# Kernel optimization log

Hardware: AMD Instinct MI355X
Metric: run time of the kernel (lower is better)

## Reference

```python
import jax, jax.numpy as jnp
import numpy as np

B, K, V = 32, 2048, 60000
D, H, L, NB = 512, 8, 4, 5
DH, M = D // H, 256  # dim_head, num random features
EPS_K = 1e-4


def _ln(x, g, b, eps=1e-5):
    mu = x.mean(-1, keepdims=True)
    var = ((x - mu) ** 2).mean(-1, keepdims=True)
    return (x - mu) / jnp.sqrt(var + eps) * g + b


def _favor_feats(x, proj, is_query):
    # FAVOR+ positive softmax-kernel features (lucidrains performer)
    dn = x.shape[-1] ** -0.25
    xd = x * dn
    dd = jnp.einsum('bhnd,md->bhnm', xd, proj)
    diag = 0.5 * jnp.sum(xd * xd, -1, keepdims=True)
    mx = jnp.max(dd, -1, keepdims=True) if is_query else jnp.max(dd)
    return (proj.shape[0] ** -0.5) * (jnp.exp(dd - diag - mx) + EPS_K)


def _orth_proj(m, d, rng):
    # gaussian orthogonal random matrix (scaling=0: chi row norms)
    blocks = []
    for _ in range(-(-m // d)):
        q, _ = np.linalg.qr(rng.standard_normal((d, d)))
        blocks.append(q.T)
    mat = np.concatenate(blocks)[:m]
    mult = np.linalg.norm(rng.standard_normal((m, d)), axis=1)
    return (mult[:, None] * mat).astype(np.float32)


def setup_inputs() -> dict:
    rng = np.random.default_rng(0)
    w = lambda *s: jnp.asarray(rng.standard_normal(s).astype(np.float32) * 0.02)
    return dict(
        expr=jnp.asarray(rng.random((B, K)).astype(np.float32)),
        coords=jnp.asarray(rng.standard_normal((B, 2)).astype(np.float32)),
        gene_ids=jnp.arange(K, dtype=jnp.int32),
        gene_table=w(V, D), pos_table=w(K, D), value_table=w(NB, D),
        sp_w=w(2, D), sp_b=jnp.zeros(D), sp_ln_g=jnp.ones(D), sp_ln_b=jnp.zeros(D),
        ln1_g=jnp.ones((L, D)), ln1_b=jnp.zeros((L, D)),
        qw=w(L, D, D), qb=jnp.zeros((L, D)), kw=w(L, D, D), kb=jnp.zeros((L, D)),
        vw=w(L, D, D), vb=jnp.zeros((L, D)), ow=w(L, D, D), ob=jnp.zeros((L, D)),
        proj=jnp.asarray(np.stack([_orth_proj(M, DH, rng) for _ in range(L)])),
        ln2_g=jnp.ones((L, D)), ln2_b=jnp.zeros((L, D)),
        ff1_w=w(L, D, 4 * D), ff1_b=jnp.zeros((L, 4 * D)),
        ff2_w=w(L, 4 * D, D), ff2_b=jnp.zeros((L, D)),
        cq_w=w(D, D), cq_b=jnp.zeros(D), ck_w=w(D, D), ck_b=jnp.zeros(D),
        cv_w=w(D, D), cv_b=jnp.zeros(D), co_w=w(D, D), co_b=jnp.zeros(D),
    )


def reference(expr, coords, gene_ids, gene_table, pos_table, value_table,
              sp_w, sp_b, sp_ln_g, sp_ln_b, ln1_g, ln1_b, qw, qb, kw, kb,
              vw, vb, ow, ob, proj, ln2_g, ln2_b, ff1_w, ff1_b, ff2_w, ff2_b,
              cq_w, cq_b, ck_w, ck_b, cv_w, cv_b, co_w, co_b):
    b, k = expr.shape
    bins = jnp.clip((expr * NB).astype(jnp.int32), 0, NB - 1)
    gene_embeds = gene_table[gene_ids][None] + pos_table[None, :k] + value_table[bins]
    sp = jax.nn.gelu(_ln(coords @ sp_w + sp_b, sp_ln_g, sp_ln_b), approximate=False)
    x = jnp.concatenate([sp[:, None, :], gene_embeds], axis=1)  # (B, K+1, D)
    n = k + 1
    for l in range(L):
        h = _ln(x, ln1_g[l], ln1_b[l])
        q = (h @ qw[l] + qb[l]).reshape(b, n, H, DH).transpose(0, 2, 1, 3)
        kk = (h @ kw[l] + kb[l]).reshape(b, n, H, DH).transpose(0, 2, 1, 3)
        v = (h @ vw[l] + vb[l]).reshape(b, n, H, DH).transpose(0, 2, 1, 3)
        qp = _favor_feats(q, proj[l], True)   # (b,h,n,M)
        kp = _favor_feats(kk, proj[l], False)
        dinv = 1.0 / jnp.einsum('bhnm,bhm->bhn', qp, kp.sum(axis=2))
        ctx = jnp.einsum('bhnm,bhnd->bhmd', kp, v)
        o = jnp.einsum('bhnm,bhmd->bhnd', qp, ctx) * dinv[..., None]
        o = o.transpose(0, 2, 1, 3).reshape(b, n, D)
        x = x + (o @ ow[l] + ob[l])
        h = _ln(x, ln2_g[l], ln2_b[l])
        x = x + jax.nn.gelu(h @ ff1_w[l] + ff1_b[l], approximate=False) @ ff2_w[l] + ff2_b[l]
    qc = x[:, :1] @ cq_w + cq_b
    kc = x[:, 1:] @ ck_w + ck_b
    vc = x[:, 1:] @ cv_w + cv_b
    attn = jax.nn.softmax(jnp.einsum('bqd,bkd->bqk', qc, kc) / (D ** 0.5), axis=-1)
    pooled = jnp.einsum('bqk,bkd->bqd', attn, vc)[:, 0]
    return pooled @ co_w + co_b
```

## Files before the change

### kernel.cpp

```cpp
#include <hip/hip_runtime.h>
#include <hip/hip_bf16.h>

#define BB 32
#define KK 2048
#define NTOK 2049
#define DD 512
#define NH 8
#define DHD 64
#define NL 4
#define MM 256
#define RTOT (BB*NTOK)
#define HROWS (RTOT/2)
#define DN 0.35355339059327373f
#define RM 0.0625f
#define EPSK 1e-4f

typedef __attribute__((ext_vector_type(8))) short bf16x8;
typedef __attribute__((ext_vector_type(4))) float f32x4;

__device__ __forceinline__ float wsum(float v) {
#pragma unroll
  for (int o = 32; o; o >>= 1) v += __shfl_xor(v, o);
  return v;
}
__device__ __forceinline__ float wmax(float v) {
#pragma unroll
  for (int o = 32; o; o >>= 1) v = fmaxf(v, __shfl_xor(v, o));
  return v;
}
__device__ __forceinline__ float gelu1(float v) {
  return 0.5f * v * (1.0f + erff(v * 0.70710678118654752f));
}
__device__ __forceinline__ float b2f(unsigned short u) {
  union { unsigned int i; float f; } w; w.i = ((unsigned int)u) << 16; return w.f;
}
__device__ __forceinline__ unsigned short f2b(float f) {
  union { float f; unsigned int i; } w; w.f = f;
  unsigned int r = w.i + 0x7FFFu + ((w.i >> 16) & 1u);
  return (unsigned short)(r >> 16);
}
__device__ __forceinline__ float4 ld4(const float* p) { return *(const float4*)p; }
__device__ __forceinline__ float4 ld4(const unsigned short* p) {
  ushort4 u = *(const ushort4*)p;
  return make_float4(b2f(u.x), b2f(u.y), b2f(u.z), b2f(u.w));
}
__device__ __forceinline__ void st4(float* p, float4 v) { *(float4*)p = v; }
__device__ __forceinline__ void st4(unsigned short* p, float4 v) {
  ushort4 u; u.x = f2b(v.x); u.y = f2b(v.y); u.z = f2b(v.z); u.w = f2b(v.w);
  *(ushort4*)p = u;
}
__device__ __forceinline__ bf16x8 ld8s(const unsigned short* p) {
  union { ushort4 u[2]; bf16x8 v; } w;
  w.u[0] = *(const ushort4*)p;
  w.u[1] = *(const ushort4*)(p + 4);
  return w.v;
}
__device__ __forceinline__ void gload16(const void* g, void* l) {
  __builtin_amdgcn_global_load_lds(
      (const __attribute__((address_space(1))) void*)g,
      (__attribute__((address_space(3))) void*)l, 16, 0, 0);
}

__global__ void sentinel_k(float* out, int n) {
  int i = blockIdx.x * 256 + threadIdx.x;
  if (i < n) out[i] = 12345.0f;
}

__global__ void biaspack_k(const float* __restrict__ a, const float* __restrict__ bsrc,
                           float* __restrict__ dst) {
  int i = threadIdx.x;
  dst[i] = a[i]; dst[i + 256] = a[i + 256];
  dst[512 + i] = bsrc[i]; dst[768 + i] = bsrc[i + 256];
}
__global__ void biaspack3_k(const float* __restrict__ a, const float* __restrict__ bsrc,
                            const float* __restrict__ c, float* __restrict__ dst) {
  int i = threadIdx.x;
  dst[i] = a[i]; dst[i + 256] = a[i + 256];
  dst[512 + i] = bsrc[i]; dst[768 + i] = bsrc[i + 256];
  dst[1024 + i] = c[i]; dst[1280 + i] = c[i + 256];
}

__global__ __launch_bounds__(256) void wcvt_k(const float* __restrict__ W,
    unsigned short* __restrict__ Wt, int Kd, int Cols) {
  __shared__ float Ls[64][65];
  int tid = threadIdx.x;
  int n0 = blockIdx.x * 64, k0 = blockIdx.y * 64;
  int kr = tid >> 2, nseg = (tid & 3) << 4;
#pragma unroll
  for (int u = 0; u < 4; ++u) {
    float4 v = *(const float4*)(W + (size_t)(k0 + kr) * Cols + n0 + nseg + u * 4);
    *(float4*)&Ls[kr][nseg + u * 4] = v;
  }
  __syncthreads();
  int nr = tid >> 2, kseg = (tid & 3) << 4;
  unsigned int pk[8];
#pragma unroll
  for (int i = 0; i < 8; ++i) {
    unsigned short lo = f2b(Ls[kseg + 2 * i][nr]);
    unsigned short hi = f2b(Ls[kseg + 2 * i + 1][nr]);
    pk[i] = (unsigned int)lo | ((unsigned int)hi << 16);
  }
  unsigned short* dst = Wt + (size_t)(n0 + nr) * Kd + k0 + kseg;
  ((uint4*)dst)[0] = make_uint4(pk[0], pk[1], pk[2], pk[3]);
  ((uint4*)dst)[1] = make_uint4(pk[4], pk[5], pk[6], pk[7]);
}

__global__ __launch_bounds__(256) void embed_k(const float* __restrict__ expr,
    const int* __restrict__ gene_ids, const float* __restrict__ gene_table,
    const float* __restrict__ pos_table, const float* __restrict__ value_tab,
    unsigned short* __restrict__ x) {
  int tok = blockIdx.x * 2 + (threadIdx.x >> 7);
  int t = threadIdx.x & 127;
  int b = tok >> 11;
  int k = tok & 2047;
  float e = expr[tok];
  int bin = (int)(e * 5.0f);
  bin = bin < 0 ? 0 : (bin > 4 ? 4 : bin);
  int g = gene_ids[k];
  float4 a = ((const float4*)(gene_table + (size_t)g * DD))[t];
  float4 p = ((const float4*)(pos_table + (size_t)k * DD))[t];
  float4 vv = ((const float4*)(value_tab + (size_t)bin * DD))[t];
  float4 r;
  r.x = a.x + p.x + vv.x; r.y = a.y + p.y + vv.y;
  r.z = a.z + p.z + vv.z; r.w = a.w + p.w + vv.w;
  st4(x + ((size_t)b * NTOK + 1 + k) * DD + t * 4, r);
}

__global__ __launch_bounds__(256) void sp_k(const float* __restrict__ coords,
    const float* __restrict__ sp_w, const float* __restrict__ sp_b,
    const float* __restrict__ g, const float* __restrict__ bb,
    unsigned short* __restrict__ x) {
  int b = blockIdx.x, t = threadIdx.x;
  __shared__ float red[8];
  float c0 = coords[2 * b], c1 = coords[2 * b + 1];
  float v0 = fmaf(c0, sp_w[t],       fmaf(c1, sp_w[512 + t], sp_b[t]));
  float v1 = fmaf(c0, sp_w[t + 256], fmaf(c1, sp_w[768 + t], sp_b[t + 256]));
  float s = wsum(v0 + v1);
  int wid = t >> 6;
  if ((t & 63) == 0) red[wid] = s;
  __syncthreads();
  float mu = (red[0] + red[1] + red[2] + red[3]) * (1.0f / 512.0f);
  float d0 = v0 - mu, d1 = v1 - mu;
  float s2 = wsum(d0 * d0 + d1 * d1);
  if ((t & 63) == 0) red[4 + wid] = s2;
  __syncthreads();
  float var = (red[4] + red[5] + red[6] + red[7]) * (1.0f / 512.0f);
  float rs = rsqrtf(var + 1e-5f);
  float y0 = d0 * rs * g[t] + bb[t];
  float y1 = d1 * rs * g[t + 256] + bb[t + 256];
  x[(size_t)b * NTOK * DD + t] = f2b(gelu1(y0));
  x[(size_t)b * NTOK * DD + t + 256] = f2b(gelu1(y1));
}

__global__ __launch_bounds__(128) void ln_k(const unsigned short* __restrict__ x,
    const float* __restrict__ gamma, const float* __restrict__ beta,
    unsigned short* __restrict__ h) {
  size_t row = blockIdx.x;
  int t = threadIdx.x;
  float4 v = ld4(x + row * DD + t * 4);
  float s = v.x + v.y + v.z + v.w;
  float s2 = v.x * v.x + v.y * v.y + v.z * v.z + v.w * v.w;
  __shared__ float red[4];
  float ws1 = wsum(s), ws2 = wsum(s2);
  int wid = t >> 6;
  if ((t & 63) == 0) { red[wid * 2] = ws1; red[wid * 2 + 1] = ws2; }
  __syncthreads();
  float S = red[0] + red[2], S2 = red[1] + red[3];
  float mu = S * (1.0f / 512.0f);
  float var = S2 * (1.0f / 512.0f) - mu * mu;
  float rs = rsqrtf(var + 1e-5f);
  float4 gm = ((const float4*)gamma)[t], bt = ((const float4*)beta)[t];
  float4 o;
  o.x = (v.x - mu) * rs * gm.x + bt.x;
  o.y = (v.y - mu) * rs * gm.y + bt.y;
  o.z = (v.z - mu) * rs * gm.z + bt.z;
  o.w = (v.w - mu) * rs * gm.w + bt.w;
  st4(h + row * DD + t * 4, o);
}

template <typename TC, int FLAGS>
__global__ __launch_bounds__(256) void gemm_bb(const unsigned short* __restrict__ A, long lda,
    const unsigned short* __restrict__ Wt, const float* __restrict__ bias,
    TC* __restrict__ C, int ldc, int R, int Kd) {
  __shared__ unsigned short Sh[128 * 136];
  unsigned short* As = Sh;
  unsigned short* Bs = Sh + 128 * 64;
  const int tid = threadIdx.x;
  const int lane = tid & 63;
  const int w = tid >> 6;
  const int wr = w >> 1, wc = w & 1;
  const int nwg = gridDim.x * gridDim.y;
  const int orig = blockIdx.y * gridDim.x + blockIdx.x;
  const int qd = nwg >> 3, rm = nwg & 7;
  const int xcd = orig & 7, idx = orig >> 3;
  const int wg = (xcd < rm ? xcd * (qd + 1) : rm * (qd + 1) + (xcd - rm) * qd) + idx;
  const int rblk = (wg / gridDim.x) << 7;
  const int cblk = (wg % gridDim.x) << 7;
  const int m0 = lane & 15, kb = lane >> 4;
  const int lrow8 = lane >> 3;
  const int csw = (((lane & 7) ^ lrow8) << 3);
  f32x4 acc[4][4] = {};
  for (int k0 = 0; k0 < Kd; k0 += 64) {
#pragma unroll
    for (int rd = 0; rd < 4; ++rd) {
      int rg = w * 32 + rd * 8;
      int gra = rblk + rg + lrow8; if (gra >= R) gra = R - 1;
      gload16(A  + (size_t)gra * lda + k0 + csw, &As[rg * 64]);
      gload16(Wt + (size_t)(cblk + rg + lrow8) * Kd + k0 + csw, &Bs[rg * 64]);
    }
    __syncthreads();
    bf16x8 af[2][4], bfr[2][4];
#pragma unroll
    for (int ks = 0; ks < 2; ++ks) {
      int c = (ks << 2) | kb;
#pragma unroll
      for (int mi = 0; mi < 4; ++mi) {
        int ar = wr * 64 + mi * 16 + m0;
        af[ks][mi] = *(const bf16x8*)&As[ar * 64 + ((c ^ (ar & 7)) << 3)];
        int br = wc * 64 + mi * 16 + m0;
        bfr[ks][mi] = *(const bf16x8*)&Bs[br * 64 + ((c ^ (br & 7)) << 3)];
      }
    }
#pragma unroll
    for (int ks = 0; ks < 2; ++ks)
#pragma unroll
      for (int mi = 0; mi < 4; ++mi)
#pragma unroll
        for (int ni = 0; ni < 4; ++ni)
          acc[mi][ni] = __builtin_amdgcn_mfma_f32_16x16x32_bf16(af[ks][mi], bfr[ks][ni], acc[mi][ni], 0, 0, 0);
    __syncthreads();
  }
  const int lrow4 = (lane >> 4) << 2, lcol = lane & 15;
  if constexpr (sizeof(TC) == 2 && (FLAGS & 2) == 0) {
#pragma unroll
    for (int mi = 0; mi < 4; ++mi)
#pragma unroll
      for (int reg = 0; reg < 4; ++reg) {
        int rloc = wr * 64 + mi * 16 + lrow4 + reg;
#pragma unroll
        for (int ni = 0; ni < 4; ++ni) {
          int cloc = wc * 64 + ni * 16 + lcol;
          float v = acc[mi][ni][reg] + bias[cblk + cloc];
          if constexpr ((FLAGS & 1) != 0) v = gelu1(v);
          Sh[rloc * 136 + cloc] = f2b(v);
        }
      }
    __syncthreads();
    int rl = tid >> 1;
    int row = rblk + rl;
    if (row < R) {
      unsigned short* cp = (unsigned short*)C + (size_t)row * ldc + cblk;
#pragma unroll
      for (int u = 0; u < 8; ++u) {
        int c = (tid & 1) * 8 + u * 16;
        *(uint4*)(cp + c) = *(const uint4*)&Sh[rl * 136 + c];
      }
    }
  } else {
    float* Sf = (float*)Sh;
#pragma unroll
    for (int p = 0; p < 2; ++p) {
      if (wr == p) {
#pragma unroll
        for (int mi = 0; mi < 4; ++mi)
#pragma unroll
          for (int reg = 0; reg < 4; ++reg) {
            int rloc = mi * 16 + lrow4 + reg;
#pragma unroll
            for (int ni = 0; ni < 4; ++ni) {
              int cloc = wc * 64 + ni * 16 + lcol;
              float v = acc[mi][ni][reg] + bias[cblk + cloc];
              if constexpr ((FLAGS & 1) != 0) v = gelu1(v);
              Sf[rloc * 132 + cloc] = v;
            }
          }
      }
      __syncthreads();
      int rl = tid >> 2;
      int row = rblk + p * 64 + rl;
      if (row < R) {
        if constexpr (sizeof(TC) == 4) {
          float* cp = (float*)C + (size_t)row * ldc + cblk;
#pragma unroll
          for (int u = 0; u < 8; ++u) {
            int c = (tid & 3) * 4 + u * 16;
            float4 nv = *(const float4*)&Sf[rl * 132 + c];
            if constexpr ((FLAGS & 2) != 0) {
              float4 old = *(const float4*)(cp + c);
              nv.x += old.x; nv.y += old.y; nv.z += old.z; nv.w += old.w;
            }
            *(float4*)(cp + c) = nv;
          }
        } else {
          unsigned short* cp = (unsigned short*)C + (size_t)row * ldc + cblk;
#pragma unroll
          for (int u = 0; u < 8; ++u) {
            int c = (tid & 3) * 4 + u * 16;
            float4 nv = *(const float4*)&Sf[rl * 132 + c];
            ushort4 old = *(const ushort4*)(cp + c);
            ushort4 nw;
            nw.x = f2b(nv.x + b2f(old.x)); nw.y = f2b(nv.y + b2f(old.y));
            nw.z = f2b(nv.z + b2f(old.z)); nw.w = f2b(nv.w + b2f(old.w));
            *(ushort4*)(cp + c) = nw;
          }
        }
      }
      __syncthreads();
    }
  }
}

template <typename TA, typename TC>
__global__ __launch_bounds__(256) void gemm_t(const TA* __restrict__ A, long lda,
    const float* __restrict__ W, const float* __restrict__ bias,
    TC* __restrict__ C, int ldc, int R, int Kd, int Cols) {
  __shared__ float As[16][68];
  __shared__ float Ws[16][64];
  int tid = threadIdx.x;
  int tx = tid & 15, ty = tid >> 4;
  int rblk = blockIdx.y << 6, cblk = blockIdx.x << 6;
  float acc[4][4] = {};
  int lr = tid >> 2, lk = (tid & 3) << 2;
  int wk = tid >> 4, wcc = (tid & 15) << 2;
  int gra = rblk + lr;
  for (int k0 = 0; k0 < Kd; k0 += 16) {
    float4 av = make_float4(0.f, 0.f, 0.f, 0.f);
    if (gra < R) av = ld4(A + (size_t)gra * lda + k0 + lk);
    As[lk][lr] = av.x; As[lk + 1][lr] = av.y; As[lk + 2][lr] = av.z; As[lk + 3][lr] = av.w;
    *(float4*)&Ws[wk][wcc] = *(const float4*)(W + (size_t)(k0 + wk) * Cols + cblk + wcc);
    __syncthreads();
#pragma unroll
    for (int p = 0; p < 16; ++p) {
      float4 a4 = *(const float4*)&As[p][ty << 2];
      float4 b4 = *(const float4*)&Ws[p][tx << 2];
      acc[0][0] = fmaf(a4.x, b4.x, acc[0][0]); acc[0][1] = fmaf(a4.x, b4.y, acc[0][1]);
      acc[0][2] = fmaf(a4.x, b4.z, acc[0][2]); acc[0][3] = fmaf(a4.x, b4.w, acc[0][3]);
      acc[1][0] = fmaf(a4.y, b4.x, acc[1][0]); acc[1][1] = fmaf(a4.y, b4.y, acc[1][1]);
      acc[1][2] = fmaf(a4.y, b4.z, acc[1][2]); acc[1][3] = fmaf(a4.y, b4.w, acc[1][3]);
      acc[2][0] = fmaf(a4.z, b4.x, acc[2][0]); acc[2][1] = fmaf(a4.z, b4.y, acc[2][1]);
      acc[2][2] = fmaf(a4.z, b4.z, acc[2][2]); acc[2][3] = fmaf(a4.z, b4.w, acc[2][3]);
      acc[3][0] = fmaf(a4.w, b4.x, acc[3][0]); acc[3][1] = fmaf(a4.w, b4.y, acc[3][1]);
      acc[3][2] = fmaf(a4.w, b4.z, acc[3][2]); acc[3][3] = fmaf(a4.w, b4.w, acc[3][3]);
    }
    __syncthreads();
  }
  int gcb = cblk + (tx << 2);
  float4 bi = *(const float4*)(bias + gcb);
#pragma unroll
  for (int i = 0; i < 4; ++i) {
    int gr = rblk + (ty << 2) + i;
    if (gr < R) {
      float4 val;
      val.x = acc[i][0] + bi.x; val.y = acc[i][1] + bi.y;
      val.z = acc[i][2] + bi.z; val.w = acc[i][3] + bi.w;
      TC* cp = C + (size_t)gr * ldc + gcb;
      st4(cp, val);
    }
  }
}

__global__ __launch_bounds__(256) void kmax_k(const unsigned short* __restrict__ kv,
    const unsigned short* __restrict__ projb, float* __restrict__ bmax) {
  int orig = blockIdx.y * gridDim.x + blockIdx.x;
  int wg = ((orig & 7) << 7) + (orig >> 3);
  int bh = wg >> 2, gy = wg & 3;
  int b = bh >> 3, hh = bh & 7;
  int tid = threadIdx.x;
  int lane = tid & 63, w = tid >> 6;
  int m0 = lane & 15, kb = lane >> 4;
  __shared__ float red[4];
  bf16x8 bp[4][2];
#pragma unroll
  for (int nf = 0; nf < 4; ++nf)
#pragma unroll
    for (int ks = 0; ks < 2; ++ks)
      bp[nf][ks] = *(const bf16x8*)(projb + (size_t)(w * 64 + nf * 16 + m0) * 64 + ks * 32 + kb * 8);
  const unsigned short* kvb = kv + (size_t)b * NTOK * 1536 + hh * 64;
  float mx = -1e30f;
  for (int t = gy; t < 65; t += 4) {
    int n0 = t * 32;
    bf16x8 aq[2][2];
#pragma unroll
    for (int mi = 0; mi < 2; ++mi) {
      int n = n0 + mi * 16 + m0; if (n >= NTOK) n = NTOK - 1;
#pragma unroll
      for (int ks = 0; ks < 2; ++ks)
        aq[mi][ks] = *(const bf16x8*)(kvb + (size_t)n * 1536 + ks * 32 + kb * 8);
    }
    f32x4 da[2][4] = {};
#pragma unroll
    for (int ks = 0; ks < 2; ++ks)
#pragma unroll
      for (int mi = 0; mi < 2; ++mi)
#pragma unroll
        for (int nf = 0; nf < 4; ++nf)
          da[mi][nf] = __builtin_amdgcn_mfma_f32_16x16x32_bf16(aq[mi][ks], bp[nf][ks], da[mi][nf], 0, 0, 0);
#pragma unroll
    for (int mi = 0; mi < 2; ++mi)
#pragma unroll
      for (int nf = 0; nf < 4; ++nf)
#pragma unroll
        for (int r = 0; r < 4; ++r)
          mx = fmaxf(mx, da[mi][nf][r]);
  }
  mx *= DN;
  mx = wmax(mx);
  if ((tid & 63) == 0) red[tid >> 6] = mx;
  __syncthreads();
  if (tid == 0)
    bmax[(size_t)bh * 4 + gy] = fmaxf(fmaxf(red[0], red[1]), fmaxf(red[2], red[3]));
}

__global__ __launch_bounds__(256) void maxred_k(const float* __restrict__ in, int n,
                                                float* __restrict__ out) {
  float m = -1e30f;
  for (int i = threadIdx.x; i < n; i += 256) m = fmaxf(m, in[i]);
  m = wmax(m);
  __shared__ float red[4];
  if ((threadIdx.x & 63) == 0) red[threadIdx.x >> 6] = m;
  __syncthreads();
  if (threadIdx.x == 0) out[0] = fmaxf(fmaxf(red[0], red[1]), fmaxf(red[2], red[3]));
}

__global__ __launch_bounds__(256) void k2_k(const unsigned short* __restrict__ kv,
    const unsigned short* __restrict__ projb,
    const float* __restrict__ kmaxg, unsigned short* __restrict__ ctxTb,
    float* __restrict__ kpsum) {
  int orig = blockIdx.y * gridDim.x + blockIdx.x;
  int wg = ((orig & 7) << 7) + (orig >> 3);
  int bh = wg >> 2, mg = wg & 3;
  int b = bh >> 3, hh = bh & 7;
  int tid = threadIdx.x;
  int lane = tid & 63, w = tid >> 6;
  int m0 = lane & 15, kb = lane >> 4;
  __shared__ __align__(16) unsigned short kpT[64 * 44];
  __shared__ __align__(16) unsigned short VT[64 * 44];
  float kmax = kmaxg[0];
  bf16x8 bp[2];
#pragma unroll
  for (int ks = 0; ks < 2; ++ks)
    bp[ks] = *(const bf16x8*)(projb + (size_t)(mg * 64 + w * 16 + m0) * 64 + ks * 32 + kb * 8);
  f32x4 acc[4] = {};
  float ksum = 0.f;
  int dv = tid & 63, tq = tid >> 6;
  const unsigned short* kvb = kv + (size_t)b * NTOK * 1536 + hh * 64;
  for (int t = 0; t < 65; ++t) {
    int n0 = t * 32;
    int tlim = NTOK - n0; if (tlim > 32) tlim = 32;
    __syncthreads();
    {
      unsigned int pk[4];
#pragma unroll
      for (int j = 0; j < 8; ++j) {
        int n = n0 + tq * 8 + j; if (n >= NTOK) n = NTOK - 1;
        unsigned int v = kvb[(size_t)n * 1536 + 512 + dv];
        if (j & 1) pk[j >> 1] |= v << 16; else pk[j >> 1] = v;
      }
      *(uint2*)&VT[dv * 44 + tq * 8]     = make_uint2(pk[0], pk[1]);
      *(uint2*)&VT[dv * 44 + tq * 8 + 4] = make_uint2(pk[2], pk[3]);
    }
    bf16x8 aq[2][2];
    float dg[2];
#pragma unroll
    for (int mi = 0; mi < 2; ++mi) {
      int n = n0 + mi * 16 + m0; if (n >= NTOK) n = NTOK - 1;
      float s = 0.f;
#pragma unroll
      for (int ks = 0; ks < 2; ++ks) {
        aq[mi][ks] = *(const bf16x8*)(kvb + (size_t)n * 1536 + ks * 32 + kb * 8);
        const unsigned short* ap = (const unsigned short*)&aq[mi][ks];
#pragma unroll
        for (int j = 0; j < 8; ++j) { float v = b2f(ap[j]); s = fmaf(v, v, s); }
      }
      s += __shfl_xor(s, 16);
      s += __shfl_xor(s, 32);
      dg[mi] = 0.5f * DN * DN * s;
    }
    f32x4 da[2] = {};
#pragma unroll
    for (int ks = 0; ks < 2; ++ks)
#pragma unroll
      for (int mi = 0; mi < 2; ++mi)
        da[mi] = __builtin_amdgcn_mfma_f32_16x16x32_bf16(aq[mi][ks], bp[ks], da[mi], 0, 0, 0);
#pragma unroll
    for (int mi = 0; mi < 2; ++mi) {
      unsigned int pk[2];
#pragma unroll
      for (int r = 0; r < 4; ++r) {
        float dval = __shfl(dg[mi], (kb << 2) | r);
        int tt = mi * 16 + (kb << 2) + r;
        float kp = 0.f;
        if (tt < tlim)
          kp = RM * (__expf(da[mi][r] * DN - dval - kmax) + EPSK);
        ksum += kp;
        unsigned int h = (unsigned int)f2b(kp);
        if (r & 1) pk[r >> 1] |= h << 16; else pk[r >> 1] = h;
      }
      *(uint2*)&kpT[(w * 16 + m0) * 44 + mi * 16 + (kb << 2)] = make_uint2(pk[0], pk[1]);
    }
    __syncthreads();
    bf16x8 af = ld8s(&kpT[(w * 16 + m0) * 44 + kb * 8]);
#pragma unroll
    for (int di = 0; di < 4; ++di) {
      bf16x8 bfv = ld8s(&VT[(di * 16 + m0) * 44 + kb * 8]);
      acc[di] = __builtin_amdgcn_mfma_f32_16x16x32_bf16(af, bfv, acc[di], 0, 0, 0);
    }
  }
  ksum += __shfl_xor(ksum, 16);
  ksum += __shfl_xor(ksum, 32);
  if (kb == 0) kpsum[(size_t)bh * MM + mg * 64 + w * 16 + m0] = ksum;
  unsigned short* cT = ctxTb + (size_t)bh * (64 * 256);
#pragma unroll
  for (int di = 0; di < 4; ++di)
#pragma unroll
    for (int r = 0; r < 4; ++r) {
      int m = mg * 64 + w * 16 + (kb << 2) + r;
      int d = di * 16 + m0;
      cT[d * 256 + m] = f2b(acc[di][r]);
    }
}

__global__ __launch_bounds__(256) void qfeat_k(unsigned short* __restrict__ kv,
    const unsigned short* __restrict__ projb,
    const unsigned short* __restrict__ ctxTb,
    const float* __restrict__ kpsum) {
  int orig = blockIdx.y * gridDim.x + blockIdx.x;
  int wg = ((orig & 7) * 416) + (orig >> 3);
  int bh = wg / 13, gy = wg % 13;
  int b = bh >> 3, hh = bh & 7;
  int tid = threadIdx.x;
  int lane = tid & 63, w = tid >> 6;
  int m0 = lane & 15, kb = lane >> 4;
  __shared__ float ddl[32 * 266];
  __shared__ unsigned short Pb[32 * 264];
  __shared__ float ksum_s[256];
  __shared__ float diag_s[32];
  __shared__ float dinv_s[32];
  ksum_s[tid] = kpsum[(size_t)bh * MM + tid];
  bf16x8 bp[4][2], bc[8];
#pragma unroll
  for (int nf = 0; nf < 4; ++nf)
#pragma unroll
    for (int ks = 0; ks < 2; ++ks)
      bp[nf][ks] = *(const bf16x8*)(projb + (size_t)(w * 64 + nf * 16 + m0) * 64 + ks * 32 + kb * 8);
  const unsigned short* cT = ctxTb + (size_t)bh * (64 * 256);
#pragma unroll
  for (int ks = 0; ks < 8; ++ks)
    bc[ks] = *(const bf16x8*)(cT + (size_t)(w * 16 + m0) * 256 + ks * 32 + kb * 8);
  unsigned short* kvb = kv + (size_t)b * NTOK * 1536 + hh * 64;
  int t8 = tid >> 3, q8 = tid & 7;
  for (int t = gy; t < 65; t += 13) {
    int n0 = t * 32;
    int tlim = NTOK - n0; if (tlim > 32) tlim = 32;
    bf16x8 aq[2][2];
#pragma unroll
    for (int mi = 0; mi < 2; ++mi) {
      int n = n0 + mi * 16 + m0; if (n >= NTOK) n = NTOK - 1;
#pragma unroll
      for (int ks = 0; ks < 2; ++ks)
        aq[mi][ks] = *(const bf16x8*)(kvb + (size_t)n * 1536 + 1024 + ks * 32 + kb * 8);
    }
#pragma unroll
    for (int mi = 0; mi < 2; ++mi) {
      float s = 0.f;
      const unsigned short* ap = (const unsigned short*)&aq[mi][0];
#pragma unroll
      for (int j = 0; j < 16; ++j) { float v = b2f(ap[j]); s = fmaf(v, v, s); }
      s += __shfl_xor(s, 16); s += __shfl_xor(s, 32);
      if (w == 0 && kb == 0) diag_s[mi * 16 + m0] = 0.5f * DN * DN * s;
    }
    f32x4 da[2][4] = {};
#pragma unroll
    for (int ks = 0; ks < 2; ++ks)
#pragma unroll
      for (int mi = 0; mi < 2; ++mi)
#pragma unroll
        for (int nf = 0; nf < 4; ++nf)
          da[mi][nf] = __builtin_amdgcn_mfma_f32_16x16x32_bf16(aq[mi][ks], bp[nf][ks], da[mi][nf], 0, 0, 0);
#pragma unroll
    for (int mi = 0; mi < 2; ++mi)
#pragma unroll
      for (int nf = 0; nf < 4; ++nf)
#pragma unroll
        for (int r = 0; r < 4; ++r)
          ddl[(mi * 16 + kb * 4 + r) * 266 + w * 64 + nf * 16 + m0] = da[mi][nf][r] * DN;
    __syncthreads();
    float mx = -1e30f;
    if (t8 < tlim) {
      for (int j = 0; j < 32; ++j) mx = fmaxf(mx, ddl[t8 * 266 + q8 + 8 * j]);
    }
    mx = fmaxf(mx, __shfl_xor(mx, 1));
    mx = fmaxf(mx, __shfl_xor(mx, 2));
    mx = fmaxf(mx, __shfl_xor(mx, 4));
    float den = 0.f;
    if (t8 < tlim) {
      float dg = diag_s[t8];
      for (int j = 0; j < 32; ++j) {
        int mm = q8 + 8 * j;
        float e = RM * (__expf(ddl[t8 * 266 + mm] - dg - mx) + EPSK);
        Pb[t8 * 264 + mm] = f2b(e);
        den = fmaf(e, ksum_s[mm], den);
      }
    }
    den += __shfl_xor(den, 1); den += __shfl_xor(den, 2); den += __shfl_xor(den, 4);
    if (q8 == 0 && t8 < tlim) dinv_s[t8] = 1.0f / den;
    __syncthreads();
    f32x4 oa[2] = {};
#pragma unroll
    for (int ks = 0; ks < 8; ++ks)
#pragma unroll
      for (int mi = 0; mi < 2; ++mi) {
        bf16x8 ap = *(const bf16x8*)&Pb[(mi * 16 + m0) * 264 + ks * 32 + kb * 8];
        oa[mi] = __builtin_amdgcn_mfma_f32_16x16x32_bf16(ap, bc[ks], oa[mi], 0, 0, 0);
      }
#pragma unroll
    for (int mi = 0; mi < 2; ++mi)
#pragma unroll
      for (int r = 0; r < 4; ++r) {
        int row = mi * 16 + kb * 4 + r;
        if (row < tlim) {
          kvb[(size_t)(n0 + row) * 1536 + w * 16 + m0] =
              f2b(oa[mi][r] * dinv_s[row]);
        }
      }
    __syncthreads();
  }
}

__global__ __launch_bounds__(256) void attn_sc_k(const unsigned short* __restrict__ qc,
    const unsigned short* __restrict__ kcvc, float* __restrict__ scbuf,
    float* __restrict__ pmax) {
  int b = blockIdx.x, g = blockIdx.y, tid = threadIdx.x;
  int w = tid >> 6, lane = tid & 63;
  __shared__ float qs[DD];
  __shared__ float red[4];
  {
    ushort2 qu = ((const ushort2*)(qc + (size_t)b * DD))[tid];
    ((float2*)qs)[tid] = make_float2(b2f(qu.x), b2f(qu.y));
  }
  __syncthreads();
  float mx = -1e30f;
  for (int it = 0; it < 64; ++it) {
    int kk = g * 256 + w * 64 + it;
    const unsigned short* row = kcvc + ((size_t)b * NTOK + 1 + kk) * 1024 + lane * 8;
    float4 r0 = ld4(row), r1 = ld4(row + 4);
    float4 q0 = ((const float4*)qs)[lane * 2], q1 = ((const float4*)qs)[lane * 2 + 1];
    float s = r0.x * q0.x + r0.y * q0.y + r0.z * q0.z + r0.w * q0.w
            + r1.x * q1.x + r1.y * q1.y + r1.z * q1.z + r1.w * q1.w;
    s = wsum(s) * 0.044194173824159216f;
    if (lane == 0) scbuf[(size_t)b * KK + kk] = s;
    mx = fmaxf(mx, s);
  }
  if (lane == 0) red[w] = mx;
  __syncthreads();
  if (tid == 0) pmax[b * 8 + g] = fmaxf(fmaxf(red[0], red[1]), fmaxf(red[2], red[3]));
}
__global__ __launch_bounds__(256) void attn_w_k(const float* __restrict__ pmax,
    float* __restrict__ scbuf, float* __restrict__ pinv) {
  int b = blockIdx.x, tid = threadIdx.x;
  __shared__ float red[4];
  float mx = -1e30f;
#pragma unroll
  for (int i = 0; i < 8; ++i) mx = fmaxf(mx, pmax[b * 8 + i]);
  float sum = 0.f;
  for (int i = tid; i < KK; i += 256) {
    float e = __expf(scbuf[(size_t)b * KK + i] - mx);
    scbuf[(size_t)b * KK + i] = e;
    sum += e;
  }
  sum = wsum(sum);
  if ((tid & 63) == 0) red[tid >> 6] = sum;
  __syncthreads();
  if (tid == 0) pinv[b] = 1.0f / (red[0] + red[1] + red[2] + red[3]);
}
__global__ __launch_bounds__(256) void attn_vs_k(const float* __restrict__ scbuf,
    const unsigned short* __restrict__ kcvc, float* __restrict__ ppart) {
  int b = blockIdx.x, g = blockIdx.y, tid = threadIdx.x;
  float2 acc = {0.f, 0.f};
  for (int it = 0; it < 256; ++it) {
    int kk = g * 256 + it;
    float wgt = scbuf[(size_t)b * KK + kk];
    ushort2 vu = ((const ushort2*)(kcvc + ((size_t)b * NTOK + 1 + kk) * 1024 + 512))[tid];
    acc.x = fmaf(wgt, b2f(vu.x), acc.x);
    acc.y = fmaf(wgt, b2f(vu.y), acc.y);
  }
  ((float2*)(ppart + ((size_t)b * 8 + g) * DD))[tid] = acc;
}
__global__ __launch_bounds__(256) void attn_red_k(const float* __restrict__ ppart,
    const float* __restrict__ pinv, float* __restrict__ pooled) {
  int b = blockIdx.x, tid = threadIdx.x;
  float inv = pinv[b];
  float2 acc = {0.f, 0.f};
#pragma unroll
  for (int g = 0; g < 8; ++g) {
    float2 p = ((const float2*)(ppart + ((size_t)b * 8 + g) * DD))[tid];
    acc.x += p.x; acc.y += p.y;
  }
  ((float2*)(pooled + (size_t)b * DD))[tid] = make_float2(acc.x * inv, acc.y * inv);
}

__global__ __launch_bounds__(256) void out_k(const float* __restrict__ pooled,
    const float* __restrict__ co_w, const float* __restrict__ co_b,
    float* __restrict__ out) {
  int b = blockIdx.x, tid = threadIdx.x;
  __shared__ float ps[DD];
  ((float2*)ps)[tid] = ((const float2*)(pooled + (size_t)b * DD))[tid];
  __syncthreads();
  float a0 = co_b[tid], a1 = co_b[tid + 256];
  for (int d = 0; d < 512; ++d) {
    float p = ps[d];
    a0 = fmaf(p, co_w[(size_t)d * 512 + tid], a0);
    a1 = fmaf(p, co_w[(size_t)d * 512 + tid + 256], a1);
  }
  out[(size_t)b * 512 + tid] = a0;
  out[(size_t)b * 512 + tid + 256] = a1;
}

extern "C" void kernel_launch(void* const* d_in, const int* in_sizes, int n_in,
                              void* d_out, int out_size, void* d_ws, size_t ws_size,
                              hipStream_t stream) {
  const float* expr       = (const float*)d_in[0];
  const float* coords     = (const float*)d_in[1];
  const int*   gene_ids   = (const int*)d_in[2];
  const float* gene_table = (const float*)d_in[3];
  const float* pos_table  = (const float*)d_in[4];
  const float* value_tab  = (const float*)d_in[5];
  const float* sp_w  = (const float*)d_in[6];
  const float* sp_b  = (const float*)d_in[7];
  const float* sp_g  = (const float*)d_in[8];
  const float* sp_bb = (const float*)d_in[9];
  const float* ln1_g = (const float*)d_in[10];
  const float* ln1_b = (const float*)d_in[11];
  const float* qw = (const float*)d_in[12];
  const float* qbias = (const float*)d_in[13];
  const float* kw = (const float*)d_in[14];
  const float* kbias = (const float*)d_in[15];
  const float* vw = (const float*)d_in[16];
  const float* vbias = (const float*)d_in[17];
  const float* ow = (const float*)d_in[18];
  const float* obias = (const float*)d_in[19];
  const float* proj  = (const float*)d_in[20];
  const float* ln2_g = (const float*)d_in[21];
  const float* ln2_b = (const float*)d_in[22];
  const float* ff1w = (const float*)d_in[23];
  const float* ff1b = (const float*)d_in[24];
  const float* ff2w = (const float*)d_in[25];
  const float* ff2b = (const float*)d_in[26];
  const float* cqw = (const float*)d_in[27];
  const float* cqb = (const float*)d_in[28];
  const float* ckw = (const float*)d_in[29];
  const float* ckb = (const float*)d_in[30];
  const float* cvw = (const float*)d_in[31];
  const float* cvb = (const float*)d_in[32];
  const float* cow = (const float*)d_in[33];
  const float* cob = (const float*)d_in[34];
  float* out = (float*)d_out;

  const size_t SZ = (size_t)RTOT * DD;
  const size_t MS = (size_t)DD * DD;
  const size_t FS = (size_t)DD * 4 * DD;
  const size_t LST = 4 * MS + 2 * FS;
  const size_t WBN = 4 * LST + 2 * MS;
  const size_t CTXN = (size_t)BB * NH * 64 * 256;
  const size_t KVQN = (size_t)RTOT * 1536;

  unsigned short* x = (unsigned short*)d_ws;
  unsigned short* KVQb = x + SZ;
  unsigned short* Cb = KVQb + KVQN;
  unsigned short* wb = Cb + SZ;
  unsigned short* ctxTb = wb + WBN;
  unsigned short* projb = ctxTb + CTXN;
  float* kpsum = (float*)(projb + (size_t)NL * MM * DHD);
  float* pooled = kpsum + (size_t)BB * NH * MM;
  float* bmax  = pooled + (size_t)BB * DD;
  float* kmaxg = bmax + 2816;
  float* scbuf = kmaxg + 16;
  float* pmax  = scbuf + (size_t)BB * KK;
  float* pinv  = pmax + 256;
  float* ppart = pinv + 32;
  float* biasKVQ = ppart + (size_t)BB * 8 * DD;
  unsigned short* qcb = (unsigned short*)(biasKVQ + (size_t)NL * 1536 + 1024);
  size_t need = (size_t)((char*)(qcb + (size_t)BB * DD) - (char*)d_ws) + 256;
  if (ws_size < need) {
    sentinel_k<<<(out_size + 255) / 256, 256, 0, stream>>>(out, out_size);
    return;
  }

  for (int l = 0; l < NL; ++l) {
    unsigned short* wl = wb + l * LST;
    wcvt_k<<<dim3(8, 8), 256, 0, stream>>>(kw + l * MS, wl,          512, 512);
    wcvt_k<<<dim3(8, 8), 256, 0, stream>>>(vw + l * MS, wl + MS,     512, 512);
    wcvt_k<<<dim3(8, 8), 256, 0, stream>>>(qw + l * MS, wl + 2 * MS, 512, 512);
    wcvt_k<<<dim3(8, 8), 256, 0, stream>>>(ow + l * MS, wl + 3 * MS, 512, 512);
    wcvt_k<<<dim3(32, 8), 256, 0, stream>>>(ff1w + l * FS, wl + 4 * MS,      512, 2048);
    wcvt_k<<<dim3(8, 32), 256, 0, stream>>>(ff2w + l * FS, wl + 4 * MS + FS, 2048, 512);
    biaspack3_k<<<1, 256, 0, stream>>>(kbias + l * DD, vbias + l * DD, qbias + l * DD,
                                       biasKVQ + l * 1536);
  }
  wcvt_k<<<dim3(8, 8), 256, 0, stream>>>(ckw, wb + 4 * LST,      512, 512);
  wcvt_k<<<dim3(8, 8), 256, 0, stream>>>(cvw, wb + 4 * LST + MS, 512, 512);
  biaspack_k<<<1, 256, 0, stream>>>(ckb, cvb, biasKVQ + NL * 1536);
  {
    const float* p4 = proj;
    unsigned short* pb = projb;
    (void)p4; (void)pb;
  }
  {
    struct Cvt { };
  }
  extern __global__ void cvtp_k(const float*, unsigned short*, size_t);
  cvtp_k<<<32, 256, 0, stream>>>(proj, projb, (size_t)NL * MM * DHD / 8);

  embed_k<<<BB * KK / 2, 256, 0, stream>>>(expr, gene_ids, gene_table, pos_table, value_tab, x);
  sp_k<<<BB, 256, 0, stream>>>(coords, sp_w, sp_b, sp_g, sp_bb, x);

  const int RB = (RTOT + 127) / 128;
  const int HB = (HROWS + 127) / 128;
  for (int l = 0; l < NL; ++l) {
    unsigned short* wl = wb + l * LST;
    const unsigned short* pbl = projb + (size_t)l * MM * DHD;
    ln_k<<<RTOT, 128, 0, stream>>>(x, ln1_g + l * DD, ln1_b + l * DD, Cb);
    gemm_bb<unsigned short, 0><<<dim3(12, RB), 256, 0, stream>>>(Cb, DD,
        wl, biasKVQ + l * 1536, KVQb, 1536, RTOT, DD);
    kmax_k<<<dim3(256, 4), 256, 0, stream>>>(KVQb, pbl, bmax);
    maxred_k<<<1, 256, 0, stream>>>(bmax, BB * NH * 4, kmaxg);
    k2_k<<<dim3(256, 4), 256, 0, stream>>>(KVQb, pbl, kmaxg, ctxTb, kpsum);
    qfeat_k<<<dim3(256, 13), 256, 0, stream>>>(KVQb, pbl, ctxTb, kpsum);
    gemm_bb<unsigned short, 2><<<dim3(4, RB), 256, 0, stream>>>(KVQb, 1536,
        wl + 3 * MS, obias + l * DD, x, DD, RTOT, DD);
    ln_k<<<RTOT, 128, 0, stream>>>(x, ln2_g + l * DD, ln2_b + l * DD, Cb);
    for (int c = 0; c < 2; ++c) {
      gemm_bb<unsigned short, 1><<<dim3(16, HB), 256, 0, stream>>>(Cb + (size_t)c * HROWS * DD, DD,
          wl + 4 * MS, ff1b + (size_t)l * 4 * DD, KVQb, 2048, HROWS, DD);
      gemm_bb<unsigned short, 2><<<dim3(4, HB), 256, 0, stream>>>(KVQb, 2048,
          wl + 4 * MS + FS, ff2b + l * DD, x + (size_t)c * HROWS * DD, DD, HROWS, 2048);
    }
  }
  gemm_bb<unsigned short, 0><<<dim3(8, RB), 256, 0, stream>>>(x, DD,
      wb + 4 * LST, biasKVQ + NL * 1536, KVQb, 1024, RTOT, DD);
  gemm_t<unsigned short, unsigned short><<<dim3(8, 1), 256, 0, stream>>>(x, (long)NTOK * DD,
      cqw, cqb, qcb, DD, BB, DD, DD);
  attn_sc_k<<<dim3(BB, 8), 256, 0, stream>>>(qcb, KVQb, scbuf, pmax);
  attn_w_k<<<BB, 256, 0, stream>>>(pmax, scbuf, pinv);
  attn_vs_k<<<dim3(BB, 8), 256, 0, stream>>>(scbuf, KVQb, ppart);
  attn_red_k<<<BB, 256, 0, stream>>>(ppart, pinv, pooled);
  out_k<<<BB, 256, 0, stream>>>(pooled, cow, cob, out);
}

__global__ __launch_bounds__(256) void cvtp_k(const float* __restrict__ src,
    unsigned short* __restrict__ dst, size_t n8) {
  size_t i = (size_t)blockIdx.x * 256 + threadIdx.x;
  if (i >= n8) return;
  float4 a = ((const float4*)src)[2 * i];
  float4 b = ((const float4*)src)[2 * i + 1];
  st4(dst + i * 8, a);
  st4(dst + i * 8 + 4, b);
}
```

Before: 5.058 ms.

## Add 256x256-tile bf16 MFMA GEMM with XCD-aware remap for QKV and FF1

Adds a new GEMM kernel with 512-thread blocks computing 256x256 output tiles using bf16 MFMA, swizzled LDS layout, and a block-index remap that groups work per XCD. It replaces the 128-tile GEMM for the QKV projection, FF1 (with GELU) and the final K/V projection, to raise arithmetic intensity per loaded tile and improve L2 locality. It also stages output through LDS for coalesced stores. Costs: larger register footprint (128 accumulator floats per thread), lower occupancy, no double buffering of global loads, and fewer blocks in flight.

```diff
diff --git a/kernel.cpp b/kernel.cpp
--- a/kernel.cpp
+++ b/kernel.cpp
@@ -307,6 +307,90 @@
       }
       __syncthreads();
     }
+  }
+}
+
+template <int FLAGS>
+__global__ __launch_bounds__(512) void gemm_bb2(const unsigned short* __restrict__ A, long lda,
+    const unsigned short* __restrict__ Wt, const float* __restrict__ bias,
+    unsigned short* __restrict__ C, int ldc, int R, int Kd) {
+  __shared__ unsigned short Sh[128 * 264];
+  unsigned short* As = Sh;
+  unsigned short* Bs = Sh + 256 * 64;
+  const int tid = threadIdx.x;
+  const int lane = tid & 63;
+  const int w = tid >> 6;
+  const int wr = w >> 2, wc = w & 3;
+  const int nwg = gridDim.x * gridDim.y;
+  const int orig = blockIdx.y * gridDim.x + blockIdx.x;
+  const int qd = nwg >> 3, rm = nwg & 7;
+  const int xcd = orig & 7, idx = orig >> 3;
+  const int wg = (xcd < rm ? xcd * (qd + 1) : rm * (qd + 1) + (xcd - rm) * qd) + idx;
+  const int rblk = (wg / gridDim.x) << 8;
+  const int cblk = (wg % gridDim.x) << 8;
+  const int m0 = lane & 15, kb = lane >> 4;
+  const int lrow8 = lane >> 3;
+  const int csw = (((lane & 7) ^ lrow8) << 3);
+  f32x4 acc[8][4] = {};
+  for (int k0 = 0; k0 < Kd; k0 += 64) {
+#pragma unroll
+    for (int rd = 0; rd < 4; ++rd) {
+      int rg = w * 32 + rd * 8;
+      int gra = rblk + rg + lrow8; if (gra >= R) gra = R - 1;
+      gload16(A  + (size_t)gra * lda + k0 + csw, &As[rg * 64]);
+      gload16(Wt + (size_t)(cblk + rg + lrow8) * Kd + k0 + csw, &Bs[rg * 64]);
+    }
+    __syncthreads();
+#pragma unroll
+    for (int ks = 0; ks < 2; ++ks) {
+      int c = (ks << 2) | kb;
+      bf16x8 af[8], bfr[4];
+#pragma unroll
+      for (int mi = 0; mi < 8; ++mi) {
+        int ar = wr * 128 + mi * 16 + m0;
+        af[mi] = *(const bf16x8*)&As[ar * 64 + ((c ^ (ar & 7)) << 3)];
+      }
+#pragma unroll
+      for (int ni = 0; ni < 4; ++ni) {
+        int br = wc * 64 + ni * 16 + m0;
+        bfr[ni] = *(const bf16x8*)&Bs[br * 64 + ((c ^ (br & 7)) << 3)];
+      }
+#pragma unroll
+      for (int mi = 0; mi < 8; ++mi)
+#pragma unroll
+        for (int ni = 0; ni < 4; ++ni)
+          acc[mi][ni] = __builtin_amdgcn_mfma_f32_16x16x32_bf16(af[mi], bfr[ni], acc[mi][ni], 0, 0, 0);
+    }
+    __syncthreads();
+  }
+  const int lrow4 = (lane >> 4) << 2, lcol = lane & 15;
+#pragma unroll
+  for (int hp = 0; hp < 2; ++hp) {
+    if (wr == hp) {
+#pragma unroll
+      for (int mi = 0; mi < 8; ++mi)
+#pragma unroll
+        for (int reg = 0; reg < 4; ++reg) {
+          int rloc = mi * 16 + lrow4 + reg;
+#pragma unroll
+          for (int ni = 0; ni < 4; ++ni) {
+            int cloc = wc * 64 + ni * 16 + lcol;
+            float v = acc[mi][ni][reg] + bias[cblk + cloc];
+            if constexpr ((FLAGS & 1) != 0) v = gelu1(v);
+            Sh[rloc * 264 + cloc] = f2b(v);
+          }
+        }
+    }
+    __syncthreads();
+    int rl = tid >> 2, qn = tid & 3;
+    int row = rblk + hp * 128 + rl;
+    if (row < R) {
+      unsigned short* cp = C + (size_t)row * ldc + cblk + qn * 64;
+#pragma unroll
+      for (int u = 0; u < 8; ++u)
+        *(uint4*)(cp + u * 8) = *(const uint4*)&Sh[rl * 264 + qn * 64 + u * 8];
+    }
+    __syncthreads();
   }
 }
 
@@ -800,14 +884,6 @@
   wcvt_k<<<dim3(8, 8), 256, 0, stream>>>(ckw, wb + 4 * LST,      512, 512);
   wcvt_k<<<dim3(8, 8), 256, 0, stream>>>(cvw, wb + 4 * LST + MS, 512, 512);
   biaspack_k<<<1, 256, 0, stream>>>(ckb, cvb, biasKVQ + NL * 1536);
-  {
-    const float* p4 = proj;
-    unsigned short* pb = projb;
-    (void)p4; (void)pb;
-  }
-  {
-    struct Cvt { };
-  }
   extern __global__ void cvtp_k(const float*, unsigned short*, size_t);
   cvtp_k<<<32, 256, 0, stream>>>(proj, projb, (size_t)NL * MM * DHD / 8);
 
@@ -815,12 +891,15 @@
   sp_k<<<BB, 256, 0, stream>>>(coords, sp_w, sp_b, sp_g, sp_bb, x);
 
   const int RB = (RTOT + 127) / 128;
+  const int RB2 = (RTOT + 255) / 256;
   const int HB = (HROWS + 127) / 128;
+  const int HB2 = (HROWS + 255) / 256;
+  (void)HB;
   for (int l = 0; l < NL; ++l) {
     unsigned short* wl = wb + l * LST;
     const unsigned short* pbl = projb + (size_t)l * MM * DHD;
     ln_k<<<RTOT, 128, 0, stream>>>(x, ln1_g + l * DD, ln1_b + l * DD, Cb);
-    gemm_bb<unsigned short, 0><<<dim3(12, RB), 256, 0, stream>>>(Cb, DD,
+    gemm_bb2<0><<<dim3(6, RB2), 512, 0, stream>>>(Cb, DD,
         wl, biasKVQ + l * 1536, KVQb, 1536, RTOT, DD);
     kmax_k<<<dim3(256, 4), 256, 0, stream>>>(KVQb, pbl, bmax);
     maxred_k<<<1, 256, 0, stream>>>(bmax, BB * NH * 4, kmaxg);
@@ -830,13 +909,13 @@
         wl + 3 * MS, obias + l * DD, x, DD, RTOT, DD);
     ln_k<<<RTOT, 128, 0, stream>>>(x, ln2_g + l * DD, ln2_b + l * DD, Cb);
     for (int c = 0; c < 2; ++c) {
-      gemm_bb<unsigned short, 1><<<dim3(16, HB), 256, 0, stream>>>(Cb + (size_t)c * HROWS * DD, DD,
+      gemm_bb2<1><<<dim3(8, HB2), 512, 0, stream>>>(Cb + (size_t)c * HROWS * DD, DD,
           wl + 4 * MS, ff1b + (size_t)l * 4 * DD, KVQb, 2048, HROWS, DD);
       gemm_bb<unsigned short, 2><<<dim3(4, HB), 256, 0, stream>>>(KVQb, 2048,
           wl + 4 * MS + FS, ff2b + l * DD, x + (size_t)c * HROWS * DD, DD, HROWS, 2048);
     }
   }
-  gemm_bb<unsigned short, 0><<<dim3(8, RB), 256, 0, stream>>>(x, DD,
+  gemm_bb2<0><<<dim3(4, RB2), 512, 0, stream>>>(x, DD,
       wb + 4 * LST, biasKVQ + NL * 1536, KVQb, 1024, RTOT, DD);
   gemm_t<unsigned short, unsigned short><<<dim3(8, 1), 256, 0, stream>>>(x, (long)NTOK * DD,
       cqw, cqb, qcb, DD, BB, DD, DD);
```

New measurement: 8.972 ms. 1.77x slower.
